# Kernel tuning notes

Measured on AMD Instinct MI355X. Metric: run time of the kernel, lower is better.

The kernel has to match this reference:

```python
import jax, jax.numpy as jnp
import numpy as np

IMG = 512; P = 16; C = 3; DIM = 512; DEPTH = 2; HEADS = 8; HD = DIM // HEADS
MLP = 2048; W = 64; NCLS = 1000; B = 8
NPATCH = (IMG // P) ** 2          # 1024
N0 = NPATCH + 1                    # 1025 tokens incl CLS
PAD = (-N0) % (2 * W)              # pad to multiple of 2w (sliding_chunks)
N = N0 + PAD                       # 1152


def _ln(x, w, b):
    m = x.mean(-1, keepdims=True)
    v = jnp.mean((x - m) ** 2, -1, keepdims=True)
    return (x - m) * jax.lax.rsqrt(v + 1e-5) * w + b


def _heads(t):
    b, n, _ = t.shape
    return t.reshape(b, n, HEADS, HD).transpose(0, 2, 1, 3)  # b h n d


def _attn(x, mask, wq, bq, wk, bk, wv, bv, wqg, bqg, wkg, bkg, wvg, bvg):
    b, n, _ = x.shape
    sc = 1.0 / np.sqrt(HD)
    q = _heads(x @ wq + bq) * sc
    k = _heads(x @ wk + bk)
    v = _heads(x @ wv + bv)
    nc = n // W
    qc = q.reshape(b, HEADS, nc, W, HD)

    def chunk3(t):  # gather prev/self/next chunk of keys/values: b h nc 3W d
        tc = t.reshape(b, HEADS, nc, W, HD)
        z = jnp.zeros_like(tc[:, :, :1])
        prev = jnp.concatenate([z, tc[:, :, :-1]], 2)
        nxt = jnp.concatenate([tc[:, :, 1:], z], 2)
        return jnp.concatenate([prev, tc, nxt], 3)

    k3, v3 = chunk3(k), chunk3(v)
    band = jnp.einsum('bhcqd,bhckd->bhcqk', qc, k3)  # b h nc W 3W
    qi = jnp.arange(W)[:, None]
    kk = jnp.arange(3 * W)[None, :]
    rel_ok = jnp.abs(kk - W - qi) <= W               # exact +-w band
    kglob = jnp.arange(nc)[:, None, None] * W + (kk - W)[None]  # nc 1 3W
    in_rng = (kglob >= 0) & (kglob < n)
    kmask = mask[jnp.clip(kglob, 0, n - 1)]
    # keep only real local keys: exclude pad (0) and global (2, handled by gcol)
    keep = rel_ok[None] & in_rng & (kmask == 1.0)    # nc W 3W
    band = jnp.where(keep[None, None], band, -1e9)
    gcol = jnp.einsum('bhnd,bhd->bhn', q, k[:, :, 0])  # attend to global CLS key
    scores = jnp.concatenate([gcol[..., None], band.reshape(b, HEADS, n, 3 * W)], -1)
    a = jax.nn.softmax(scores, -1)                   # b h n (1+3W)
    out = jnp.einsum('bhcqk,bhckd->bhcqd', a[..., 1:].reshape(b, HEADS, nc, W, 3 * W), v3)
    out = out.reshape(b, HEADS, n, HD) + a[..., 0:1] * v[:, :, 0:1]
    # global CLS row attends to everything with its own projections
    qg0 = ((x[:, 0] @ wqg + bqg) * sc).reshape(b, HEADS, HD)
    kg = _heads(x @ wkg + bkg)
    vg = _heads(x @ wvg + bvg)
    gs = jnp.where(mask[None, None] > 0, jnp.einsum('bhd,bhnd->bhn', qg0, kg), -1e9)
    gout = jnp.einsum('bhn,bhnd->bhd', jax.nn.softmax(gs, -1), vg)
    out = out.at[:, :, 0].set(gout)
    return out.transpose(0, 2, 1, 3).reshape(b, n, DIM)


def setup_inputs():
    key = jax.random.key(0)
    ks = iter(jax.random.split(key, 20))

    def w(shape, s=0.02):
        return jax.random.normal(next(ks), shape, jnp.float32) * s

    return {
        'img': jax.random.normal(next(ks), (B, C, IMG, IMG), jnp.float32),
        'patch_w': w((P * P * C, DIM)), 'patch_b': jnp.zeros((DIM,), jnp.float32),
        'cls_tok': jax.random.uniform(next(ks), (1, 1, DIM), jnp.float32),
        'pos_emb': w((1, N0, DIM), 1.0),
        'ln1_w': jnp.ones((DEPTH, DIM), jnp.float32), 'ln1_b': jnp.zeros((DEPTH, DIM), jnp.float32),
        'wq': w((DEPTH, DIM, DIM)), 'bq': jnp.zeros((DEPTH, DIM), jnp.float32),
        'wk': w((DEPTH, DIM, DIM)), 'bk': jnp.zeros((DEPTH, DIM), jnp.float32),
        'wv': w((DEPTH, DIM, DIM)), 'bv': jnp.zeros((DEPTH, DIM), jnp.float32),
        'wqg': w((DEPTH, DIM, DIM)), 'bqg': jnp.zeros((DEPTH, DIM), jnp.float32),
        'wkg': w((DEPTH, DIM, DIM)), 'bkg': jnp.zeros((DEPTH, DIM), jnp.float32),
        'wvg': w((DEPTH, DIM, DIM)), 'bvg': jnp.zeros((DEPTH, DIM), jnp.float32),
        'ln2_w': jnp.ones((DEPTH, DIM), jnp.float32), 'ln2_b': jnp.zeros((DEPTH, DIM), jnp.float32),
        'w1': w((DEPTH, DIM, MLP)), 'b1': jnp.zeros((DEPTH, MLP), jnp.float32),
        'w2': w((DEPTH, MLP, DIM)), 'b2': jnp.zeros((DEPTH, DIM), jnp.float32),
        'head_ln_w': jnp.ones((DIM,), jnp.float32), 'head_ln_b': jnp.zeros((DIM,), jnp.float32),
        'head_w': w((DIM, NCLS)), 'head_b': jnp.zeros((NCLS,), jnp.float32),
    }


def reference(img, patch_w, patch_b, cls_tok, pos_emb, ln1_w, ln1_b, wq, bq, wk, bk,
              wv, bv, wqg, bqg, wkg, bkg, wvg, bvg, ln2_w, ln2_b, w1, b1, w2, b2,
              head_ln_w, head_ln_b, head_w, head_b):
    b = img.shape[0]
    hh = IMG // P
    # b c (h p1) (w p2) -> b (h w) (p1 p2 c)
    x = img.reshape(b, C, hh, P, hh, P).transpose(0, 2, 4, 3, 5, 1).reshape(b, hh * hh, P * P * C)
    x = x @ patch_w + patch_b
    x = jnp.concatenate([jnp.broadcast_to(cls_tok, (b, 1, DIM)), x], 1) + pos_emb
    x = jnp.pad(x, ((0, 0), (0, PAD), (0, 0)))
    mask = jnp.zeros((N,), jnp.float32).at[:N0].set(1.0).at[0].set(2.0)
    for i in range(DEPTH):
        x = x + _attn(_ln(x, ln1_w[i], ln1_b[i]), mask,
                      wq[i], bq[i], wk[i], bk[i], wv[i], bv[i],
                      wqg[i], bqg[i], wkg[i], bkg[i], wvg[i], bvg[i])
        h = jax.nn.gelu(_ln(x, ln2_w[i], ln2_b[i]) @ w1[i] + b1[i], approximate=False)
        x = x + h @ w2[i] + b2[i]
    cls = x[:, 0]  # pool='cls'
    return _ln(cls, head_ln_w, head_ln_b) @ head_w + head_b
```

## Files before the change

kernel.cpp:

```cpp
#include <hip/hip_runtime.h>
#include <hip/hip_bf16.h>
#include <math.h>

typedef __hip_bfloat16 bf16;
typedef float f32x4 __attribute__((ext_vector_type(4)));
typedef short s16x8 __attribute__((ext_vector_type(8)));
typedef short s16x4 __attribute__((ext_vector_type(4)));
typedef unsigned int u32;
typedef unsigned long long u64;

#define NB 8
#define NROW 1025
#define MTOT (NB*NROW)
#define DIMD 512
#define NHEAD 8
#define HD 64
#define MLPD 2048
#define QKVN 2560
#define JSTR 1032

__device__ __forceinline__ float b2f(short u) {
    return __builtin_bit_cast(float, (u32)(unsigned short)u << 16);
}
__device__ __forceinline__ unsigned short f2bfbits(float f) {
    __hip_bfloat16 h = __float2bfloat16(f);
    return __builtin_bit_cast(unsigned short, h);
}
__device__ __forceinline__ void g2lds16(const bf16* g, bf16* l) {
    __builtin_amdgcn_global_load_lds((const __attribute__((address_space(1))) u32*)g,
                                     (__attribute__((address_space(3))) u32*)l, 16, 0, 0);
}

__global__ __launch_bounds__(256) void transpose_cvt_L(
    const float* __restrict__ src, bf16* __restrict__ dst, int K, int N, float scale)
{
    __shared__ float t[32][33];
    const int z = blockIdx.z;
    const float* s = src + (size_t)z * K * N;
    bf16* d = dst + (size_t)z * N * K;
    const int n0 = blockIdx.x * 32, k0 = blockIdx.y * 32;
    const int tx = threadIdx.x, ty = threadIdx.y;
#pragma unroll
    for (int i = 0; i < 32; i += 8)
        t[ty + i][tx] = s[(long)(k0 + ty + i) * N + n0 + tx];
    __syncthreads();
#pragma unroll
    for (int i = 0; i < 32; i += 8)
        d[(long)(n0 + ty + i) * K + k0 + tx] = __float2bfloat16(t[tx][ty + i] * scale);
}

__global__ __launch_bounds__(256) void qkvw_t(
    const float* __restrict__ wq, const float* __restrict__ wk, const float* __restrict__ wv,
    const float* __restrict__ wkg, const float* __restrict__ wvg, bf16* __restrict__ qkvT)
{
    __shared__ float t[32][33];
    const int z = blockIdx.z, L = z / 5, s = z % 5;
    const float* srcs[5] = {wq, wk, wv, wkg, wvg};
    const float* src = srcs[s] + (size_t)L * DIMD * DIMD;
    bf16* dst = qkvT + ((size_t)L * QKVN + s * DIMD) * DIMD;
    const float scale = (s == 0) ? 0.125f : 1.f;
    const int n0 = blockIdx.x * 32, k0 = blockIdx.y * 32;
    const int tx = threadIdx.x, ty = threadIdx.y;
#pragma unroll
    for (int i = 0; i < 32; i += 8)
        t[ty + i][tx] = src[(long)(k0 + ty + i) * DIMD + n0 + tx];
    __syncthreads();
#pragma unroll
    for (int i = 0; i < 32; i += 8)
        dst[(long)(n0 + ty + i) * DIMD + k0 + tx] = __float2bfloat16(t[tx][ty + i] * scale);
}

__global__ __launch_bounds__(256) void build_bias(
    const float* __restrict__ bq, const float* __restrict__ bk, const float* __restrict__ bv,
    const float* __restrict__ bkg, const float* __restrict__ bvg, float* __restrict__ outb)
{
    int idx = blockIdx.x * 256 + threadIdx.x;
    if (idx >= 2 * QKVN) return;
    int L = idx / QKVN, c = idx % QKVN;
    int sec = c >> 9, d = c & 511;
    const float* src = (sec == 0) ? bq : (sec == 1) ? bk : (sec == 2) ? bv : (sec == 3) ? bkg : bvg;
    float v = src[L * DIMD + d];
    if (sec == 0) v *= 0.125f;
    outb[idx] = v;
}

__global__ __launch_bounds__(256) void im2col(
    const float* __restrict__ img, bf16* __restrict__ A)
{
    const int idx = blockIdx.x * 256 + threadIdx.x;
    const int pp = idx & 7;
    const int pw = (idx >> 3) & 31;
    const int py = (idx >> 8) & 15;
    const int ph = (idx >> 12) & 31;
    const int b  = idx >> 17;
    const int hh = ph * 16 + py;
    const int w  = pw * 16 + pp * 2;
    const float2 c0 = *(const float2*)(img + (((long)(b * 3 + 0) * 512 + hh) * 512 + w));
    const float2 c1 = *(const float2*)(img + (((long)(b * 3 + 1) * 512 + hh) * 512 + w));
    const float2 c2 = *(const float2*)(img + (((long)(b * 3 + 2) * 512 + hh) * 512 + w));
    const long row = (long)b * 1024 + ph * 32 + pw;
    u32* dst = (u32*)(A + row * 768 + py * 48 + pp * 6);
    dst[0] = (u32)f2bfbits(c0.x) | ((u32)f2bfbits(c1.x) << 16);
    dst[1] = (u32)f2bfbits(c2.x) | ((u32)f2bfbits(c0.y) << 16);
    dst[2] = (u32)f2bfbits(c1.y) | ((u32)f2bfbits(c2.y) << 16);
}

__global__ __launch_bounds__(256) void cls_row(
    const float* __restrict__ cls, const float* __restrict__ pos, float* __restrict__ x)
{
    const int idx = blockIdx.x * 256 + threadIdx.x;
    const int b = idx >> 9, d = idx & 511;
    x[(long)b * NROW * DIMD + d] = cls[d] + pos[d];
}

__global__ __launch_bounds__(256) void ln_fwd(
    const float* __restrict__ x, const float* __restrict__ w,
    const float* __restrict__ bb, bf16* __restrict__ y, int Mrows)
{
    const int row = blockIdx.x * 4 + (threadIdx.x >> 6);
    if (row >= Mrows) return;
    const int lane = threadIdx.x & 63;
    const float* xr = x + (long)row * DIMD + lane * 8;
    float4 a = *(const float4*)xr;
    float4 b4 = *(const float4*)(xr + 4);
    float s  = a.x + a.y + a.z + a.w + b4.x + b4.y + b4.z + b4.w;
    float sq = a.x*a.x + a.y*a.y + a.z*a.z + a.w*a.w + b4.x*b4.x + b4.y*b4.y + b4.z*b4.z + b4.w*b4.w;
#pragma unroll
    for (int o = 32; o; o >>= 1) { s += __shfl_xor(s, o); sq += __shfl_xor(sq, o); }
    float mean = s * (1.f / 512.f);
    float rstd = rsqrtf(sq * (1.f / 512.f) - mean * mean + 1e-5f);
    bf16* yr = y + (long)row * DIMD + lane * 8;
    const float* wp = w + lane * 8;
    const float* bp = bb + lane * 8;
    float vals[8] = {a.x, a.y, a.z, a.w, b4.x, b4.y, b4.z, b4.w};
#pragma unroll
    for (int u = 0; u < 8; ++u)
        yr[u] = __float2bfloat16((vals[u] - mean) * rstd * wp[u] + bp[u]);
}

template<int EPI>
__global__ __launch_bounds__(256) void gemm128(
    const bf16* __restrict__ A, const bf16* __restrict__ Bt,
    const float* __restrict__ bias,
    float* __restrict__ Cf, bf16* __restrict__ Cb,
    int M, int N, int K, const float* __restrict__ posp, bf16* __restrict__ vTout)
{
    __shared__ bf16 aL[2][128 * 64];
    __shared__ bf16 bL[2][128 * 64];
    const int tid = threadIdx.x, lane = tid & 63, w = tid >> 6;
    const int m0 = blockIdx.y * 128, n0 = blockIdx.x * 128;
    const int wm = w >> 1, wn = w & 1;
    f32x4 acc[4][4] = {};
    const int nk = K >> 6;
    const int srow = lane >> 3;
    const int scol = ((lane & 7) ^ srow) * 8;

#define STAGE(buf, kt) do {                                                        \
        _Pragma("unroll")                                                          \
        for (int i = 0; i < 4; ++i) {                                              \
            const int rb = i * 32 + w * 8;                                         \
            long ar = m0 + rb + srow; if (ar >= M) ar = M - 1;                     \
            g2lds16(A  + ar * (long)K + (long)(kt) * 64 + scol, &aL[buf][rb * 64]);\
            g2lds16(Bt + (long)(n0 + rb + srow) * K + (long)(kt) * 64 + scol,      \
                    &bL[buf][rb * 64]);                                            \
        } } while (0)

    STAGE(0, 0);
    __syncthreads();
    int cur = 0;
    const int fr = lane & 15;
    const int lc0 = lane >> 4;
    const int px = lane & 7;
    const int arow_b = (wm * 64 + fr) << 7;
    const int brow_b = (wn * 64 + fr) << 7;
    for (int kt = 0; kt < nk; ++kt) {
        if (kt + 1 < nk) STAGE(cur ^ 1, kt + 1);
        const char* aP = (const char*)&aL[cur][0];
        const char* bP = (const char*)&bL[cur][0];
#pragma unroll
        for (int ksub = 0; ksub < 2; ++ksub) {
            const int cb = ((ksub * 4 + lc0) ^ px) << 4;
            s16x8 af[4], bf_[4];
#pragma unroll
            for (int mi = 0; mi < 4; ++mi) af[mi]  = *(const s16x8*)(aP + arow_b + mi * 2048 + cb);
#pragma unroll
            for (int ni = 0; ni < 4; ++ni) bf_[ni] = *(const s16x8*)(bP + brow_b + ni * 2048 + cb);
#pragma unroll
            for (int mi = 0; mi < 4; ++mi)
#pragma unroll
                for (int ni = 0; ni < 4; ++ni)
                    acc[mi][ni] = __builtin_amdgcn_mfma_f32_16x16x32_bf16(af[mi], bf_[ni], acc[mi][ni], 0, 0, 0);
        }
        __syncthreads();
        cur ^= 1;
    }
#undef STAGE
    const int lr = (lane >> 4) * 4, lc = lane & 15;
#pragma unroll
    for (int mi = 0; mi < 4; ++mi) {
        const int gr0 = m0 + wm * 64 + mi * 16 + lr;
#pragma unroll
        for (int ni = 0; ni < 4; ++ni) {
            const int gc = n0 + wn * 64 + ni * 16 + lc;
            const float bv = bias[gc];
            if (EPI == 1) {
                unsigned short pk[4];
#pragma unroll
                for (int j = 0; j < 4; ++j) {
                    const int gr = gr0 + j;
                    if (gr < M) {
                        bf16 hv = __float2bfloat16(acc[mi][ni][j] + bv);
                        Cb[(long)gr * N + gc] = hv;
                        pk[j] = __builtin_bit_cast(unsigned short, hv);
                    } else pk[j] = 0;
                }
                if (gc >= 1024 && gc < 1536) {
                    const int d = gc - 1024;
                    const int bb2 = gr0 / NROW, jj = gr0 - bb2 * NROW;
                    if (jj <= 1021 && gr0 + 3 < M) {
                        u64 pack =  (u64)pk[0] | ((u64)pk[1] << 16)
                                 | ((u64)pk[2] << 32) | ((u64)pk[3] << 48);
                        *(u64*)&vTout[((long)bb2 * 512 + d) * JSTR + jj] = pack;
                    } else {
#pragma unroll
                        for (int j = 0; j < 4; ++j) {
                            const int gr = gr0 + j;
                            if (gr < M) {
                                const int b3 = gr / NROW, j3 = gr - b3 * NROW;
                                vTout[((long)b3 * 512 + d) * JSTR + j3] =
                                    __builtin_bit_cast(bf16, pk[j]);
                            }
                        }
                    }
                }
            } else {
#pragma unroll
                for (int j = 0; j < 4; ++j) {
                    const int gr = gr0 + j;
                    if (gr < M) {
                        float v = acc[mi][ni][j] + bv;
                        if (EPI == 0) Cf[(long)gr * N + gc] = v;
                        else if (EPI == 2) {
                            float g = 0.5f * v * (1.f + erff(v * 0.70710678118f));
                            Cb[(long)gr * N + gc] = __float2bfloat16(g);
                        } else if (EPI == 3) {
                            Cf[(long)gr * N + gc] += v;
                        } else {
                            const int bb2 = gr >> 10, pidx = gr & 1023;
                            Cf[((long)bb2 * NROW + 1 + pidx) * DIMD + gc]
                                = v + posp[(long)(pidx + 1) * DIMD + gc];
                        }
                    }
                }
            }
        }
    }
}

__global__ __launch_bounds__(256) void band_glob_attn(
    const bf16* __restrict__ qkv, const bf16* __restrict__ vT,
    const bf16* __restrict__ ybf, const float* __restrict__ wqg,
    const float* __restrict__ bqg, float* __restrict__ x)
{
    __shared__ bf16 KlPl[193 * 72];
    __shared__ bf16 Vt[64 * 192];
    const int c = blockIdx.x, h = blockIdx.y, b = blockIdx.z;
    const int tid = threadIdx.x, lane = tid & 63, w = tid >> 6;
    const long rowb = (long)b * NROW;
    const int hoff = h * HD;

    if (c == 16) {
        float* gsh  = (float*)KlPl;
        float* y0   = gsh;
        float* P    = gsh + 512;
        float* qgs  = gsh + 1537;
        float* redx = gsh + 1601;
        for (int d = tid; d < 512; d += 256) y0[d] = __bfloat162float(ybf[rowb * DIMD + d]);
        __syncthreads();
        const int dd = tid & 63, part = tid >> 6;
        {
            float a = 0.f;
            for (int kk = part; kk < 512; kk += 4)
                a += y0[kk] * wqg[(long)kk * DIMD + hoff + dd];
            redx[tid] = a;
        }
        __syncthreads();
        if (part == 0)
            qgs[dd] = (redx[dd] + redx[64 + dd] + redx[128 + dd] + redx[192 + dd]
                       + bqg[hoff + dd]) * 0.125f;
        __syncthreads();
        for (int j = tid; j < 1025; j += 256) {
            const bf16* kr = qkv + (rowb + j) * QKVN + 1536 + hoff;
            float s = 0.f;
#pragma unroll
            for (int c8 = 0; c8 < 8; ++c8) {
                s16x8 kv = *(const s16x8*)(kr + c8 * 8);
#pragma unroll
                for (int e = 0; e < 8; ++e) s += qgs[c8 * 8 + e] * b2f(kv[e]);
            }
            P[j] = s;
        }
        __syncthreads();
        float lm = -1e30f;
        for (int j = tid; j < 1025; j += 256) lm = fmaxf(lm, P[j]);
        redx[tid] = lm; __syncthreads();
        for (int st = 128; st; st >>= 1) { if (tid < st) redx[tid] = fmaxf(redx[tid], redx[tid + st]); __syncthreads(); }
        const float mx = redx[0]; __syncthreads();
        float ls = 0.f;
        for (int j = tid; j < 1025; j += 256) { float e = __expf(P[j] - mx); P[j] = e; ls += e; }
        redx[tid] = ls; __syncthreads();
        for (int st = 128; st; st >>= 1) { if (tid < st) redx[tid] += redx[tid + st]; __syncthreads(); }
        const float invg = 1.f / redx[0];
        __syncthreads();
        float accg = 0.f;
#pragma unroll 4
        for (int j = part; j < 1025; j += 4)
            accg += P[j] * __bfloat162float(qkv[(rowb + j) * QKVN + 2048 + hoff + dd]);
        redx[tid] = accg;
        __syncthreads();
        if (part == 0)
            x[rowb * DIMD + hoff + dd] += (redx[dd] + redx[64 + dd] + redx[128 + dd] + redx[192 + dd]) * invg;
        return;
    }

    const int qi0 = 1 + c * 64, jbase = qi0 - 64;
    bf16* Kl = KlPl;

    for (int task = tid; task < 193 * 8; task += 256) {
        const int d8 = task & 7, r = task >> 3;
        int j = (r < 192) ? (jbase + r) : 0;
        j = j < 0 ? 0 : (j > 1024 ? 1024 : j);
        s16x8 val = *(const s16x8*)(qkv + (rowb + j) * QKVN + 512 + hoff + d8 * 8);
        *(s16x8*)(Kl + r * 72 + d8 * 8) = val;
    }
    for (int task = tid; task < 64 * 24; task += 256) {
        const int kc = task % 24, d = task / 24;
        int j0 = jbase + kc * 8;
        j0 = j0 < 0 ? 0 : (j0 > 1017 ? 1017 : j0);
        s16x8 v = *(const s16x8*)(vT + ((long)(b * 512 + hoff + d)) * JSTR + j0);
        const int bo = (d * 384 + kc * 16) ^ ((d & 7) << 4);
        *(s16x8*)((char*)Vt + bo) = v;
    }

    const int q = lane & 15, g = lane >> 4;
    const int qg = w * 16 + q;
    s16x8 qf0, qf1;
    {
        const bf16* qp = qkv + (rowb + qi0 + qg) * QKVN + hoff + g * 8;
        qf0 = *(const s16x8*)qp;
        qf1 = *(const s16x8*)(qp + 32);
    }
    __syncthreads();

    f32x4 sc[13] = {};
#pragma unroll
    for (int nt = 0; nt < 13; ++nt) {
        const bf16* kp = Kl + (nt * 16 + q) * 72 + g * 8;
        s16x8 k0 = *(const s16x8*)kp;
        s16x8 k1 = *(const s16x8*)(kp + 32);
        sc[nt] = __builtin_amdgcn_mfma_f32_16x16x32_bf16(k0, qf0, sc[nt], 0, 0, 0);
        sc[nt] = __builtin_amdgcn_mfma_f32_16x16x32_bf16(k1, qf1, sc[nt], 0, 0, 0);
    }

    const int lo_ = (qg > 1 - jbase) ? qg : 1 - jbase;
    const int hi_ = (qg + 128 < 1024 - jbase) ? qg + 128 : 1024 - jbase;
    float m = -1e30f;
#pragma unroll
    for (int nt = 0; nt < 12; ++nt)
#pragma unroll
        for (int j = 0; j < 4; ++j) {
            const int slot = nt * 16 + g * 4 + j;
            float s = (slot >= lo_ && slot <= hi_) ? sc[nt][j] : -1e9f;
            sc[nt][j] = s;
            m = fmaxf(m, s);
        }
#pragma unroll
    for (int j = 0; j < 4; ++j) {
        float s = (g == 0 && j == 0) ? sc[12][j] : -1e9f;
        sc[12][j] = s;
        m = fmaxf(m, s);
    }
    m = fmaxf(m, __shfl_xor(m, 16));
    m = fmaxf(m, __shfl_xor(m, 32));
    float sum = 0.f;
#pragma unroll
    for (int nt = 0; nt < 13; ++nt)
#pragma unroll
        for (int j = 0; j < 4; ++j) {
            float p = __expf(sc[nt][j] - m);
            sc[nt][j] = p;
            sum += p;
        }
    sum += __shfl_xor(sum, 16);
    sum += __shfl_xor(sum, 32);
    const float inv = 1.f / sum;
    const float a0 = __shfl(sc[12][0], q);

    __syncthreads();

    char* plw = (char*)KlPl + w * 6144;
#pragma unroll
    for (int nt = 0; nt < 12; ++nt) {
        u32 lo2 = (u32)f2bfbits(sc[nt][0]) | ((u32)f2bfbits(sc[nt][1]) << 16);
        u32 hi2 = (u32)f2bfbits(sc[nt][2]) | ((u32)f2bfbits(sc[nt][3]) << 16);
        const int bo = (q * 384 + (nt * 16 + g * 4) * 2) ^ ((q & 7) << 4);
        *(uint2*)(plw + bo) = make_uint2(lo2, hi2);
    }
    __syncthreads();

    f32x4 ac[4] = {};
#pragma unroll
    for (int ks = 0; ks < 6; ++ks) {
        const int pbo = (q * 384 + (ks * 32 + g * 8) * 2) ^ ((q & 7) << 4);
        s16x8 pf = *(const s16x8*)(plw + pbo);
#pragma unroll
        for (int mt = 0; mt < 4; ++mt) {
            const int d = mt * 16 + q;
            const int vbo = ((d * 192 + ks * 32 + g * 8) * 2) ^ ((d & 7) << 4);
            s16x8 vf = *(const s16x8*)((char*)Vt + vbo);
            ac[mt] = __builtin_amdgcn_mfma_f32_16x16x32_bf16(vf, pf, ac[mt], 0, 0, 0);
        }
    }

    const bf16* v0p = qkv + rowb * QKVN + 1024 + hoff;
    float* xr = x + (rowb + qi0 + qg) * DIMD + hoff;
#pragma unroll
    for (int mt = 0; mt < 4; ++mt) {
        const int d0 = mt * 16 + g * 4;
        const s16x4 vv = *(const s16x4*)(v0p + d0);
        float4 prev = *(float4*)(xr + d0);
        prev.x += (ac[mt][0] + a0 * b2f(vv[0])) * inv;
        prev.y += (ac[mt][1] + a0 * b2f(vv[1])) * inv;
        prev.z += (ac[mt][2] + a0 * b2f(vv[2])) * inv;
        prev.w += (ac[mt][3] + a0 * b2f(vv[3])) * inv;
        *(float4*)(xr + d0) = prev;
    }
}

__global__ __launch_bounds__(512) void lncls(
    const float* __restrict__ x, const float* __restrict__ lw,
    const float* __restrict__ lb, float* __restrict__ out)
{
    const int b = threadIdx.x >> 6, lane = threadIdx.x & 63;
    const int d0 = lane * 8;
    const float* xr = x + (long)b * NROW * DIMD + d0;
    float4 a = *(const float4*)xr;
    float4 b4 = *(const float4*)(xr + 4);
    float s  = a.x + a.y + a.z + a.w + b4.x + b4.y + b4.z + b4.w;
    float sq = a.x*a.x + a.y*a.y + a.z*a.z + a.w*a.w + b4.x*b4.x + b4.y*b4.y + b4.z*b4.z + b4.w*b4.w;
#pragma unroll
    for (int o = 32; o; o >>= 1) { s += __shfl_xor(s, o); sq += __shfl_xor(sq, o); }
    const float mean = s * (1.f / 512.f);
    const float rstd = rsqrtf(sq * (1.f / 512.f) - mean * mean + 1e-5f);
    float vals[8] = {a.x, a.y, a.z, a.w, b4.x, b4.y, b4.z, b4.w};
#pragma unroll
    for (int u = 0; u < 8; ++u)
        out[b * DIMD + d0 + u] = (vals[u] - mean) * rstd * lw[d0 + u] + lb[d0 + u];
}

__global__ __launch_bounds__(128) void head_gemv(
    const float* __restrict__ lnc, const float* __restrict__ hw,
    const float* __restrict__ hb, float* __restrict__ out)
{
    const int idx = blockIdx.x * 128 + threadIdx.x;
    if (idx >= NB * 1000) return;
    const int b = idx / 1000, cc = idx - b * 1000;
    const float* lr = lnc + b * DIMD;
    float a = hb[cc];
#pragma unroll 8
    for (int kk = 0; kk < 512; ++kk) a += lr[kk] * hw[(long)kk * 1000 + cc];
    out[idx] = a;
}

extern "C" void kernel_launch(void* const* d_in, const int* in_sizes, int n_in,
                              void* d_out, int out_size, void* d_ws, size_t ws_size,
                              hipStream_t stream)
{
    const float* img     = (const float*)d_in[0];
    const float* patch_w = (const float*)d_in[1];
    const float* patch_b = (const float*)d_in[2];
    const float* cls_tok = (const float*)d_in[3];
    const float* pos_emb = (const float*)d_in[4];
    const float* ln1_w   = (const float*)d_in[5];
    const float* ln1_b   = (const float*)d_in[6];
    const float* wq  = (const float*)d_in[7];
    const float* bq  = (const float*)d_in[8];
    const float* wk  = (const float*)d_in[9];
    const float* bk  = (const float*)d_in[10];
    const float* wv  = (const float*)d_in[11];
    const float* bv  = (const float*)d_in[12];
    const float* wqg = (const float*)d_in[13];
    const float* bqg = (const float*)d_in[14];
    const float* wkg = (const float*)d_in[15];
    const float* bkg = (const float*)d_in[16];
    const float* wvg = (const float*)d_in[17];
    const float* bvg = (const float*)d_in[18];
    const float* ln2_w = (const float*)d_in[19];
    const float* ln2_b = (const float*)d_in[20];
    const float* w1 = (const float*)d_in[21];
    const float* b1 = (const float*)d_in[22];
    const float* w2 = (const float*)d_in[23];
    const float* b2 = (const float*)d_in[24];
    const float* hlw = (const float*)d_in[25];
    const float* hlb = (const float*)d_in[26];
    const float* hw  = (const float*)d_in[27];
    const float* hb  = (const float*)d_in[28];

    char* wsb = (char*)d_ws;
    size_t o = 0;
    auto carve = [&](size_t n) { size_t r = o; o += (n + 255) & ~(size_t)255; return r; };
    float* x    = (float*)(wsb + carve((size_t)MTOT * DIMD * 4));
    bf16*  ybf  = (bf16*) (wsb + carve((size_t)MTOT * DIMD * 2));
    bf16*  qkv  = (bf16*) (wsb + carve((size_t)MTOT * QKVN * 2));
    bf16*  hbuf = (bf16*) (wsb + carve((size_t)MTOT * MLPD * 2));
    bf16*  vT   = (bf16*) (wsb + carve((size_t)NB * 512 * JSTR * 2));
    bf16*  acol = (bf16*) (wsb + carve((size_t)8192 * 768 * 2));
    bf16*  pwt  = (bf16*) (wsb + carve((size_t)512 * 768 * 2));
    bf16*  qkvT = (bf16*) (wsb + carve((size_t)2 * QKVN * DIMD * 2));
    bf16*  w1t  = (bf16*) (wsb + carve((size_t)2 * MLPD * DIMD * 2));
    bf16*  w2t  = (bf16*) (wsb + carve((size_t)2 * DIMD * MLPD * 2));
    float* catb = (float*)(wsb + carve((size_t)2 * QKVN * 4));
    float* lnc  = (float*)(wsb + carve((size_t)NB * DIMD * 4));
    (void)ws_size; (void)in_sizes; (void)n_in; (void)out_size;

    dim3 tb(32, 8);
    transpose_cvt_L<<<dim3(16, 24, 1), tb, 0, stream>>>(patch_w, pwt, 768, 512, 1.f);
    qkvw_t<<<dim3(16, 16, 10), tb, 0, stream>>>(wq, wk, wv, wkg, wvg, qkvT);
    transpose_cvt_L<<<dim3(64, 16, 2), tb, 0, stream>>>(w1, w1t, DIMD, MLPD, 1.f);
    transpose_cvt_L<<<dim3(16, 64, 2), tb, 0, stream>>>(w2, w2t, MLPD, DIMD, 1.f);
    build_bias<<<20, 256, 0, stream>>>(bq, bk, bv, bkg, bvg, catb);

    im2col<<<4096, 256, 0, stream>>>(img, acol);
    gemm128<4><<<dim3(4, 64), 256, 0, stream>>>(
        acol, pwt, patch_b, x, nullptr, 8192, 512, 768, pos_emb, nullptr);
    cls_row<<<16, 256, 0, stream>>>(cls_tok, pos_emb, x);

    for (int L = 0; L < 2; ++L) {
        ln_fwd<<<2050, 256, 0, stream>>>(x, ln1_w + L * DIMD, ln1_b + L * DIMD, ybf, MTOT);
        gemm128<1><<<dim3(QKVN/128, 65), 256, 0, stream>>>(
            ybf, qkvT + (size_t)L * QKVN * DIMD, catb + L * QKVN, nullptr, qkv,
            MTOT, QKVN, DIMD, nullptr, vT);
        band_glob_attn<<<dim3(17, NHEAD, NB), 256, 0, stream>>>(
            qkv, vT, ybf, wqg + (size_t)L * DIMD * DIMD, bqg + L * DIMD, x);
        ln_fwd<<<2050, 256, 0, stream>>>(x, ln2_w + L * DIMD, ln2_b + L * DIMD, ybf, MTOT);
        gemm128<2><<<dim3(MLPD/128, 65), 256, 0, stream>>>(
            ybf, w1t + (size_t)L * MLPD * DIMD, b1 + L * MLPD, nullptr, hbuf,
            MTOT, MLPD, DIMD, nullptr, nullptr);
        gemm128<3><<<dim3(DIMD/128, 65), 256, 0, stream>>>(
            hbuf, w2t + (size_t)L * DIMD * MLPD, b2 + L * DIMD, x, nullptr,
            MTOT, DIMD, MLPD, nullptr, nullptr);
    }
    lncls<<<1, 512, 0, stream>>>(x, hlw, hlb, lnc);
    head_gemv<<<63, 128, 0, stream>>>(lnc, hw, hb, (float*)d_out);
}
```

Before: 573.2 us.

## Split global CLS attention into key tiles with a separate merge kernel

```diff
diff --git a/kernel.cpp b/kernel.cpp
--- a/kernel.cpp
+++ b/kernel.cpp
@@ -18,6 +18,7 @@
 #define MLPD 2048
 #define QKVN 2560
 #define JSTR 1032
+#define GTILE 8
 
 __device__ __forceinline__ float b2f(short u) {
     return __builtin_bit_cast(float, (u32)(unsigned short)u << 16);
@@ -257,10 +258,25 @@
     }
 }
 
+__global__ __launch_bounds__(256) void qg_proj(
+    const bf16* __restrict__ ybf, const float* __restrict__ wqg,
+    const float* __restrict__ bqg, float* __restrict__ qg_all)
+{
+    __shared__ float y0[512];
+    const int b = blockIdx.x, tid = threadIdx.x;
+    const long rowb = (long)b * NROW;
+    for (int d = tid; d < 512; d += 256) y0[d] = __bfloat162float(ybf[rowb * DIMD + d]);
+    __syncthreads();
+    const int c = blockIdx.y * 256 + tid;
+    float a = 0.f;
+#pragma unroll 8
+    for (int kk = 0; kk < 512; ++kk) a += y0[kk] * wqg[(long)kk * DIMD + c];
+    qg_all[b * DIMD + c] = (a + bqg[c]) * 0.125f;
+}
+
 __global__ __launch_bounds__(256) void band_glob_attn(
     const bf16* __restrict__ qkv, const bf16* __restrict__ vT,
-    const bf16* __restrict__ ybf, const float* __restrict__ wqg,
-    const float* __restrict__ bqg, float* __restrict__ x)
+    const float* __restrict__ qg_all, float* __restrict__ gpart, float* __restrict__ x)
 {
     __shared__ bf16 KlPl[193 * 72];
     __shared__ bf16 Vt[64 * 192];
@@ -269,28 +285,19 @@
     const long rowb = (long)b * NROW;
     const int hoff = h * HD;
 
-    if (c == 16) {
+    if (c >= 16) {
+        const int t = c - 16;
+        const int j0 = t * 129;
+        const int len = (1025 - j0) < 129 ? (1025 - j0) : 129;
         float* gsh  = (float*)KlPl;
-        float* y0   = gsh;
-        float* P    = gsh + 512;
-        float* qgs  = gsh + 1537;
-        float* redx = gsh + 1601;
-        for (int d = tid; d < 512; d += 256) y0[d] = __bfloat162float(ybf[rowb * DIMD + d]);
+        float* S    = gsh;
+        float* qgs  = gsh + 160;
+        float* redx = gsh + 224;
+        const int dd = tid & 63, part = tid >> 6;
+        if (tid < 64) qgs[tid] = qg_all[b * DIMD + hoff + tid];
         __syncthreads();
-        const int dd = tid & 63, part = tid >> 6;
-        {
-            float a = 0.f;
-            for (int kk = part; kk < 512; kk += 4)
-                a += y0[kk] * wqg[(long)kk * DIMD + hoff + dd];
-            redx[tid] = a;
-        }
-        __syncthreads();
-        if (part == 0)
-            qgs[dd] = (redx[dd] + redx[64 + dd] + redx[128 + dd] + redx[192 + dd]
-                       + bqg[hoff + dd]) * 0.125f;
-        __syncthreads();
-        for (int j = tid; j < 1025; j += 256) {
-            const bf16* kr = qkv + (rowb + j) * QKVN + 1536 + hoff;
+        if (tid < len) {
+            const bf16* kr = qkv + (rowb + j0 + tid) * QKVN + 1536 + hoff;
             float s = 0.f;
 #pragma unroll
             for (int c8 = 0; c8 < 8; ++c8) {
@@ -298,28 +305,31 @@
 #pragma unroll
                 for (int e = 0; e < 8; ++e) s += qgs[c8 * 8 + e] * b2f(kv[e]);
             }
-            P[j] = s;
+            S[tid] = s;
         }
         __syncthreads();
         float lm = -1e30f;
-        for (int j = tid; j < 1025; j += 256) lm = fmaxf(lm, P[j]);
+        for (int j = tid; j < len; j += 256) lm = fmaxf(lm, S[j]);
         redx[tid] = lm; __syncthreads();
         for (int st = 128; st; st >>= 1) { if (tid < st) redx[tid] = fmaxf(redx[tid], redx[tid + st]); __syncthreads(); }
-        const float mx = redx[0]; __syncthreads();
+        const float mt = redx[0]; __syncthreads();
         float ls = 0.f;
-        for (int j = tid; j < 1025; j += 256) { float e = __expf(P[j] - mx); P[j] = e; ls += e; }
+        for (int j = tid; j < len; j += 256) { float e = __expf(S[j] - mt); S[j] = e; ls += e; }
         redx[tid] = ls; __syncthreads();
         for (int st = 128; st; st >>= 1) { if (tid < st) redx[tid] += redx[tid + st]; __syncthreads(); }
-        const float invg = 1.f / redx[0];
+        const float tsum = redx[0];
         __syncthreads();
-        float accg = 0.f;
+        float acc = 0.f;
 #pragma unroll 4
-        for (int j = part; j < 1025; j += 4)
-            accg += P[j] * __bfloat162float(qkv[(rowb + j) * QKVN + 2048 + hoff + dd]);
-        redx[tid] = accg;
+        for (int j = part; j < len; j += 4)
+            acc += S[j] * __bfloat162float(qkv[(rowb + j0 + j) * QKVN + 2048 + hoff + dd]);
+        redx[tid] = acc;
         __syncthreads();
-        if (part == 0)
-            x[rowb * DIMD + hoff + dd] += (redx[dd] + redx[64 + dd] + redx[128 + dd] + redx[192 + dd]) * invg;
+        if (part == 0) {
+            float* gp = gpart + ((size_t)((b * NHEAD + h) * GTILE + t)) * 66;
+            gp[2 + dd] = redx[dd] + redx[64 + dd] + redx[128 + dd] + redx[192 + dd];
+            if (dd == 0) { gp[0] = mt; gp[1] = tsum; }
+        }
         return;
     }
 
@@ -435,6 +445,26 @@
         prev.w += (ac[mt][3] + a0 * b2f(vv[3])) * inv;
         *(float4*)(xr + d0) = prev;
     }
+}
+
+__global__ __launch_bounds__(64) void glob_merge(
+    const float* __restrict__ gp, float* __restrict__ x)
+{
+    const int hb = blockIdx.x;
+    const int b = hb >> 3, h = hb & 7;
+    const int dd = threadIdx.x;
+    const float* base = gp + (size_t)hb * GTILE * 66;
+    float m = -1e30f;
+#pragma unroll
+    for (int t = 0; t < GTILE; ++t) m = fmaxf(m, base[t * 66]);
+    float sum = 0.f, acc = 0.f;
+#pragma unroll
+    for (int t = 0; t < GTILE; ++t) {
+        const float wgt = __expf(base[t * 66] - m);
+        sum += wgt * base[t * 66 + 1];
+        acc += wgt * base[t * 66 + 2 + dd];
+    }
+    x[(long)b * NROW * DIMD + h * HD + dd] += acc / sum;
 }
 
 __global__ __launch_bounds__(512) void lncls(
@@ -520,6 +550,8 @@
     bf16*  w1t  = (bf16*) (wsb + carve((size_t)2 * MLPD * DIMD * 2));
     bf16*  w2t  = (bf16*) (wsb + carve((size_t)2 * DIMD * MLPD * 2));
     float* catb = (float*)(wsb + carve((size_t)2 * QKVN * 4));
+    float* qg_all = (float*)(wsb + carve((size_t)NB * DIMD * 4));
+    float* gpart  = (float*)(wsb + carve((size_t)NB * NHEAD * GTILE * 66 * 4));
     float* lnc  = (float*)(wsb + carve((size_t)NB * DIMD * 4));
     (void)ws_size; (void)in_sizes; (void)n_in; (void)out_size;
 
@@ -540,8 +572,11 @@
         gemm128<1><<<dim3(QKVN/128, 65), 256, 0, stream>>>(
             ybf, qkvT + (size_t)L * QKVN * DIMD, catb + L * QKVN, nullptr, qkv,
             MTOT, QKVN, DIMD, nullptr, vT);
-        band_glob_attn<<<dim3(17, NHEAD, NB), 256, 0, stream>>>(
-            qkv, vT, ybf, wqg + (size_t)L * DIMD * DIMD, bqg + L * DIMD, x);
+        qg_proj<<<dim3(NB, 2), 256, 0, stream>>>(
+            ybf, wqg + (size_t)L * DIMD * DIMD, bqg + L * DIMD, qg_all);
+        band_glob_attn<<<dim3(16 + GTILE, NHEAD, NB), 256, 0, stream>>>(
+            qkv, vT, qg_all, gpart, x);
+        glob_merge<<<NB * NHEAD, 64, 0, stream>>>(gpart, x);
         ln_fwd<<<2050, 256, 0, stream>>>(x, ln2_w + L * DIMD, ln2_b + L * DIMD, ybf, MTOT);
         gemm128<2><<<dim3(MLPD/128, 65), 256, 0, stream>>>(
             ybf, w1t + (size_t)L * MLPD * DIMD, b1 + L * MLPD, nullptr, hbuf,
```

Measured after the change: 534.8 us. -6.7%, faster.
